# Performance work log

Measured on AMD Instinct MI355X. Metric: run time of the kernel, lower is better.

Reference implementation:

```python
import jax, jax.numpy as jnp
from jax import lax
import numpy as np

B, DIM, H, W = 8, 192, 128, 128
HEADS = 4


def setup_inputs() -> dict:
    key = jax.random.key(0)
    k1, k2, k3, k4 = jax.random.split(key, 4)
    x = jax.random.normal(k1, (B, DIM, H, W), dtype=jnp.float32)
    w_qkv = jax.random.normal(k2, (2 * DIM, DIM), dtype=jnp.float32) * 0.05
    w_dw = jax.random.normal(k3, (2 * DIM, 1, 3, 3), dtype=jnp.float32) * 0.1
    w_proj = jax.random.normal(k4, (DIM, DIM), dtype=jnp.float32) * 0.05
    temperature = jnp.ones((HEADS, 1, 1), dtype=jnp.float32)
    return {"x": x, "w_qkv": w_qkv, "w_dw": w_dw, "w_proj": w_proj, "temperature": temperature}


def reference(x, w_qkv, w_dw, w_proj, temperature):
    b, c, h, w = x.shape
    heads = temperature.shape[0]
    head_c = c // heads
    # 1x1 conv: dim -> 2*dim
    qkv = jnp.einsum('oc,bchw->bohw', w_qkv, x)
    # 3x3 depthwise conv over 2*dim channels
    qkv = lax.conv_general_dilated(
        qkv, w_dw, window_strides=(1, 1), padding='SAME',
        feature_group_count=2 * c,
        dimension_numbers=('NCHW', 'OIHW', 'NCHW'))
    q, v = jnp.split(qkv, 2, axis=1)
    # [b, heads, head_c, h*w]
    q = q.reshape(b, heads, head_c, h * w)
    v = v.reshape(b, heads, head_c, h * w)
    # L2-normalize q over spatial dim; k = q
    q = q / jnp.linalg.norm(q, axis=-1, keepdims=True)
    # channel-wise attention: [b, heads, head_c, head_c]
    attn = jnp.einsum('bhcn,bhdn->bhcd', q, q) * temperature[None]
    attn = jax.nn.softmax(attn, axis=-1)
    out = jnp.einsum('bhcd,bhdn->bhcn', attn, v)
    out = out.reshape(b, c, h, w)
    # 1x1 projection
    return jnp.einsum('oc,bchw->bohw', w_proj, out)
```

## Files before the change

### kernel.cpp

```cpp
#include <hip/hip_runtime.h>

#define BB 8
#define CC 192
#define C2 384
#define HH 128
#define WW 128
#define NN 16384
#define NHEADS 4
#define HC 48
#define LTK 196
#define LTK2 98

typedef float f32x4 __attribute__((ext_vector_type(4)));
typedef float f32x16 __attribute__((ext_vector_type(16)));
typedef short s16x4 __attribute__((ext_vector_type(4)));
typedef short s16x8 __attribute__((ext_vector_type(8)));
typedef unsigned short u16;
typedef u16 u16x4 __attribute__((ext_vector_type(4)));
typedef u16 u16x8 __attribute__((ext_vector_type(8)));
typedef unsigned int u32;

__device__ __forceinline__ float bfu2f(u32 u16v) {
  return __uint_as_float(u16v << 16);
}
__device__ __forceinline__ u16 f2bfu(float f) {
  u32 u = __float_as_uint(f);
  return (u16)((u + 0x7fffu + ((u >> 16) & 1u)) >> 16);
}
__device__ __forceinline__ s16x8 ldpair(const u16* p) {
  s16x4 lo = *reinterpret_cast<const s16x4*>(p);
  s16x4 hi = *reinterpret_cast<const s16x4*>(p + 16);
  return __builtin_shufflevector(lo, hi, 0, 1, 2, 3, 4, 5, 6, 7);
}
__device__ __forceinline__ s16x8 ldb64pair(const u32* p) {
  s16x4 lo = *reinterpret_cast<const s16x4*>(p);
  s16x4 hi = *reinterpret_cast<const s16x4*>(p + 2);
  return __builtin_shufflevector(lo, hi, 0, 1, 2, 3, 4, 5, 6, 7);
}

__global__ __launch_bounds__(256) void k0_wcvt(const float* __restrict__ w,
                                               u16* __restrict__ wbf) {
  const int i = (blockIdx.x * 256 + threadIdx.x) * 4;
  f32x4 v = *reinterpret_cast<const f32x4*>(&w[i]);
  u16x4 o;
  o[0] = f2bfu(v[0]); o[1] = f2bfu(v[1]); o[2] = f2bfu(v[2]); o[3] = f2bfu(v[3]);
  *reinterpret_cast<u16x4*>(&wbf[i]) = o;
}

__global__ __launch_bounds__(512, 4) void k1_qkv(
    const float* __restrict__ x, const u16* __restrict__ wbf,
    u16* __restrict__ qkv) {
  const int n0 = blockIdx.x * 128;
  const int b  = blockIdx.y;
  __shared__ u16 Xs[128 * LTK];
  u32* Xsw = reinterpret_cast<u32*>(Xs);
  const int t = threadIdx.x, lane = t & 63;
  const int wid = t >> 6, wo = wid >> 1, wn = wid & 1;
  const int l31 = lane & 31, g2 = lane >> 5;

  {
    const int nq = t & 31, cr = t >> 5;
    const int kpb = cr >> 1;
    const int jh = cr & 1;
    const int prA = 2 * nq + jh;
    const int prB = 64 + 2 * nq + jh;
    const float* xb = x + (size_t)b * CC * NN + n0 + 4 * nq;
    #pragma unroll 6
    for (int i = 0; i < 12; ++i) {
      f32x4 v = *reinterpret_cast<const f32x4*>(xb + (size_t)(cr + 16 * i) * NN);
      u32 A  = (u32)f2bfu(v[0]) | ((u32)f2bfu(v[1]) << 16);
      u32 Bp = (u32)f2bfu(v[2]) | ((u32)f2bfu(v[3]) << 16);
      u32 oA = __shfl_xor(A, 32);
      u32 oB = __shfl_xor(Bp, 32);
      u32 va, vb;
      if (jh) {
        va = (oB & 0xffffu) | (Bp << 16);
        vb = (oB >> 16) | (Bp & 0xffff0000u);
      } else {
        va = (A & 0xffffu) | (oA << 16);
        vb = (A >> 16) | (oA & 0xffff0000u);
      }
      const int col = kpb + 8 * i;
      Xsw[prA * LTK2 + col] = va;
      Xsw[prB * LTK2 + col] = vb;
    }
  }
  __syncthreads();

  const int nb2 = wn * 32;
  const u32* browE = &Xsw[(nb2 + l31) * LTK2 + 4 * g2];
  const u32* browO = &Xsw[(64 + nb2 + l31) * LTK2 + 4 * g2];

  for (int ot = 0; ot < 3; ++ot) {
    const int o0 = ot * 128;
    const u16* wr = wbf + (size_t)(o0 + wo * 32 + l31) * CC + 8 * g2;
    f32x16 accE, accO;
    #pragma unroll
    for (int e = 0; e < 16; ++e) { accE[e] = 0.f; accO[e] = 0.f; }

    s16x8 af0 = *reinterpret_cast<const s16x8*>(wr);
    s16x8 af1 = *reinterpret_cast<const s16x8*>(wr + 16);
    #pragma unroll
    for (int s = 0; s < 6; ++s) {
      s16x8 an0, an1;
      if (s < 5) {
        an0 = *reinterpret_cast<const s16x8*>(wr + (s + 1) * 32);
        an1 = *reinterpret_cast<const s16x8*>(wr + (s + 1) * 32 + 16);
      }
      s16x8 bfE0 = ldb64pair(browE + 16 * s);
      s16x8 bfE1 = ldb64pair(browE + 16 * s + 8);
      s16x8 bfO0 = ldb64pair(browO + 16 * s);
      s16x8 bfO1 = ldb64pair(browO + 16 * s + 8);
      accE = __builtin_amdgcn_mfma_f32_32x32x16_bf16(af0, bfE0, accE, 0, 0, 0);
      accO = __builtin_amdgcn_mfma_f32_32x32x16_bf16(af0, bfO0, accO, 0, 0, 0);
      accE = __builtin_amdgcn_mfma_f32_32x32x16_bf16(af1, bfE1, accE, 0, 0, 0);
      accO = __builtin_amdgcn_mfma_f32_32x32x16_bf16(af1, bfO1, accO, 0, 0, 0);
      af0 = an0; af1 = an1;
    }
    #pragma unroll
    for (int r = 0; r < 16; ++r) {
      const int row = (r & 3) + 8 * (r >> 2) + 4 * g2;
      const u32 pk = (u32)f2bfu(accE[r]) | ((u32)f2bfu(accO[r]) << 16);
      *reinterpret_cast<u32*>(
          &qkv[((size_t)b * C2 + o0 + wo * 32 + row) * NN + n0 + wn * 64 + 2 * l31]) = pk;
    }
  }
}

__global__ __launch_bounds__(256) void k2_dw(
    const u16* __restrict__ qkv, const float* __restrict__ wdw,
    u16* __restrict__ out) {
  const int gid = blockIdx.x;
  const int rb = gid & 7;
  const int plane = gid >> 3;
  const int ch = plane % C2;
  const int t = threadIdx.x;
  const int row = rb * 16 + (t >> 4);
  const int x0 = (t & 15) * 8;
  const u16* p = qkv + (size_t)plane * NN;
  const float* wv = wdw + ch * 9;
  float o[8];
  #pragma unroll
  for (int j = 0; j < 8; ++j) o[j] = 0.f;
  #pragma unroll
  for (int dy = 0; dy < 3; ++dy) {
    const int yy = row + dy - 1;
    if ((unsigned)yy < (unsigned)HH) {
      const u16* rp = p + yy * WW;
      u16x8 m = *reinterpret_cast<const u16x8*>(&rp[x0]);
      float px[10];
      px[0] = (x0 > 0) ? bfu2f(rp[x0 - 1]) : 0.f;
      px[9] = (x0 < 120) ? bfu2f(rp[x0 + 8]) : 0.f;
      #pragma unroll
      for (int j = 0; j < 8; ++j) px[j + 1] = bfu2f(m[j]);
      const float w0 = wv[dy * 3 + 0], w1 = wv[dy * 3 + 1], w2 = wv[dy * 3 + 2];
      #pragma unroll
      for (int j = 0; j < 8; ++j)
        o[j] += w0 * px[j] + w1 * px[j + 1] + w2 * px[j + 2];
    }
  }
  u16x8 ov;
  #pragma unroll
  for (int j = 0; j < 8; ++j) ov[j] = f2bfu(o[j]);
  *reinterpret_cast<u16x8*>(&out[(size_t)plane * NN + row * WW + x0]) = ov;
}

__global__ __launch_bounds__(256) void k3_gram(
    const u16* __restrict__ qkvd, float* __restrict__ gpart) {
  const int bh = blockIdx.x, b = bh >> 2, h = bh & 3;
  const int chunk = blockIdx.y;
  const int t = threadIdx.x, lane = t & 63, wv = t >> 6;
  const int l15 = lane & 15, g = lane >> 4;
  __shared__ float red[4][2304];
  const u16* qb = qkvd + ((size_t)b * C2 + h * HC) * NN;

  f32x4 acc[3][3];
  #pragma unroll
  for (int i = 0; i < 3; ++i)
    #pragma unroll
    for (int j = 0; j < 3; ++j)
      #pragma unroll
      for (int e = 0; e < 4; ++e) acc[i][j][e] = 0.f;

  const int nbase = chunk * 1024 + wv * 256;
  #pragma unroll 2
  for (int st = 0; st < 8; ++st) {
    const int n = nbase + st * 32;
    s16x8 cf[3];
    #pragma unroll
    for (int i = 0; i < 3; ++i)
      cf[i] = ldpair(qb + (size_t)(i * 16 + l15) * NN + n + 4 * g);
    #pragma unroll
    for (int i = 0; i < 3; ++i)
      #pragma unroll
      for (int j = 0; j < 3; ++j)
        acc[i][j] = __builtin_amdgcn_mfma_f32_16x16x32_bf16(cf[i], cf[j], acc[i][j], 0, 0, 0);
  }
  #pragma unroll
  for (int i = 0; i < 3; ++i)
    #pragma unroll
    for (int j = 0; j < 3; ++j)
      #pragma unroll
      for (int r = 0; r < 4; ++r)
        red[wv][(i * 16 + 4 * g + r) * 48 + j * 16 + l15] = acc[i][j][r];
  __syncthreads();
  float* gp = gpart + ((size_t)bh * 16 + chunk) * 2304;
  for (int idx = t; idx < 2304; idx += 256)
    gp[idx] = red[0][idx] + red[1][idx] + red[2][idx] + red[3][idx];
}

__global__ __launch_bounds__(256) void k4_soft(
    const float* __restrict__ gpart, const float* __restrict__ temp,
    float* __restrict__ attn) {
  const int bh = blockIdx.x;
  const int h = bh & 3;
  const int t = threadIdx.x;
  __shared__ float G[2304];
  __shared__ float rn[48];
  for (int idx = t; idx < 2304; idx += 256) {
    float s = 0.f;
    #pragma unroll
    for (int c = 0; c < 16; ++c) s += gpart[((size_t)bh * 16 + c) * 2304 + idx];
    G[idx] = s;
  }
  __syncthreads();
  if (t < 48) rn[t] = rsqrtf(G[t * 48 + t]);
  __syncthreads();
  if (t < 48) {
    const float tm = temp[h];
    float v[48];
    float mx = -1e30f;
    #pragma unroll
    for (int j = 0; j < 48; ++j) {
      v[j] = G[t * 48 + j] * rn[t] * rn[j] * tm;
      mx = fmaxf(mx, v[j]);
    }
    float s = 0.f;
    #pragma unroll
    for (int j = 0; j < 48; ++j) { v[j] = expf(v[j] - mx); s += v[j]; }
    const float inv = 1.f / s;
    #pragma unroll
    for (int j = 0; j < 48; ++j)
      attn[(size_t)bh * 2304 + t * 48 + j] = v[j] * inv;
  }
}

__global__ __launch_bounds__(192) void k5_M(
    const float* __restrict__ wproj, const float* __restrict__ attn,
    u16* __restrict__ Mbf) {
  const int o = blockIdx.x;
  const int b = blockIdx.y;
  const int d = threadIdx.x;
  const int h = d / HC, dl = d % HC;
  const float* wrow = wproj + o * CC + h * HC;
  const float* at = attn + ((size_t)(b * NHEADS + h)) * 2304;
  float s = 0.f;
  #pragma unroll
  for (int c = 0; c < HC; ++c) s = fmaf(wrow[c], at[c * HC + dl], s);
  Mbf[((size_t)b * CC + o) * CC + d] = f2bfu(s);
}

__global__ __launch_bounds__(256, 4) void k6_out(
    const u16* __restrict__ Mbf, const u16* __restrict__ qkvd,
    float* __restrict__ out) {
  const int n0 = blockIdx.x * 128;
  const int b  = blockIdx.y;
  __shared__ u16 Vs[128 * LTK];
  u32* Vsw = reinterpret_cast<u32*>(Vs);
  const int t = threadIdx.x, lane = t & 63;
  const int wid = t >> 6, wo = wid >> 1, wn = wid & 1;
  const int l31 = lane & 31, g2 = lane >> 5;

  {
    const int nq = t & 31, cr = t >> 5;
    const int kpb = cr >> 1;
    const int jh = cr & 1;
    const int prA = 2 * nq + jh;
    const int prB = 64 + 2 * nq + jh;
    const u16* vbp = qkvd + ((size_t)b * C2 + CC) * NN + n0 + 4 * nq;
    #pragma unroll 6
    for (int i = 0; i < 24; ++i) {
      u16x4 m = *reinterpret_cast<const u16x4*>(vbp + (size_t)(cr + 8 * i) * NN);
      u32 A  = (u32)m[0] | ((u32)m[1] << 16);
      u32 Bp = (u32)m[2] | ((u32)m[3] << 16);
      u32 oA = __shfl_xor(A, 32);
      u32 oB = __shfl_xor(Bp, 32);
      u32 va, vb;
      if (jh) {
        va = (oB & 0xffffu) | (Bp << 16);
        vb = (oB >> 16) | (Bp & 0xffff0000u);
      } else {
        va = (A & 0xffffu) | (oA << 16);
        vb = (A >> 16) | (oA & 0xffff0000u);
      }
      const int col = kpb + 4 * i;
      Vsw[prA * LTK2 + col] = va;
      Vsw[prB * LTK2 + col] = vb;
    }
  }
  __syncthreads();

  const int nb2 = wn * 32;
  const u32* browE = &Vsw[(nb2 + l31) * LTK2 + 4 * g2];
  const u32* browO = &Vsw[(64 + nb2 + l31) * LTK2 + 4 * g2];
  const u16* Ab = Mbf + (size_t)b * CC * CC;

  for (int ot = 0; ot < 3; ++ot) {
    const int o0 = ot * 64;
    const u16* ar = Ab + (size_t)(o0 + wo * 32 + l31) * CC + 8 * g2;
    f32x16 accE, accO;
    #pragma unroll
    for (int e = 0; e < 16; ++e) { accE[e] = 0.f; accO[e] = 0.f; }

    s16x8 af0 = *reinterpret_cast<const s16x8*>(ar);
    s16x8 af1 = *reinterpret_cast<const s16x8*>(ar + 16);
    #pragma unroll
    for (int s = 0; s < 6; ++s) {
      s16x8 an0, an1;
      if (s < 5) {
        an0 = *reinterpret_cast<const s16x8*>(ar + (s + 1) * 32);
        an1 = *reinterpret_cast<const s16x8*>(ar + (s + 1) * 32 + 16);
      }
      s16x8 bfE0 = ldb64pair(browE + 16 * s);
      s16x8 bfE1 = ldb64pair(browE + 16 * s + 8);
      s16x8 bfO0 = ldb64pair(browO + 16 * s);
      s16x8 bfO1 = ldb64pair(browO + 16 * s + 8);
      accE = __builtin_amdgcn_mfma_f32_32x32x16_bf16(af0, bfE0, accE, 0, 0, 0);
      accO = __builtin_amdgcn_mfma_f32_32x32x16_bf16(af0, bfO0, accO, 0, 0, 0);
      accE = __builtin_amdgcn_mfma_f32_32x32x16_bf16(af1, bfE1, accE, 0, 0, 0);
      accO = __builtin_amdgcn_mfma_f32_32x32x16_bf16(af1, bfO1, accO, 0, 0, 0);
      af0 = an0; af1 = an1;
    }
    #pragma unroll
    for (int r = 0; r < 16; ++r) {
      const int row = (r & 3) + 8 * (r >> 2) + 4 * g2;
      float2 st;
      st.x = accE[r];
      st.y = accO[r];
      *reinterpret_cast<float2*>(
          &out[((size_t)b * CC + o0 + wo * 32 + row) * NN + n0 + wn * 64 + 2 * l31]) = st;
    }
  }
}

extern "C" void kernel_launch(void* const* d_in, const int* in_sizes, int n_in,
                              void* d_out, int out_size, void* d_ws, size_t ws_size,
                              hipStream_t stream) {
  const float* x      = (const float*)d_in[0];
  const float* w_qkv  = (const float*)d_in[1];
  const float* w_dw   = (const float*)d_in[2];
  const float* w_proj = (const float*)d_in[3];
  const float* temp   = (const float*)d_in[4];
  float* out = (float*)d_out;

  const size_t OFF_QKV   = 0;
  const size_t OFF_QKVD  = 100663296ULL;
  const size_t OFF_GPART = 201326592ULL;
  const size_t OFF_ATTN  = 206045184ULL;
  const size_t OFF_M     = 206340096ULL;
  const size_t OFF_WBF   = 206929920ULL;
  const size_t NEEDED    = 207077376ULL;
  if (ws_size < NEEDED) return;

  char* ws = (char*)d_ws;
  u16* qkv   = (u16*)(ws + OFF_QKV);
  u16* qkvd  = (u16*)(ws + OFF_QKVD);
  float* gpart = (float*)(ws + OFF_GPART);
  float* attn  = (float*)(ws + OFF_ATTN);
  u16* Mbf   = (u16*)(ws + OFF_M);
  u16* wbf   = (u16*)(ws + OFF_WBF);

  k0_wcvt<<<dim3(72), 256, 0, stream>>>(w_qkv, wbf);
  k1_qkv <<<dim3(128, 8), 512, 0, stream>>>(x, wbf, qkv);
  k2_dw  <<<dim3(BB * C2 * 8), 256, 0, stream>>>(qkv, w_dw, qkvd);
  k3_gram<<<dim3(BB * NHEADS, 16), 256, 0, stream>>>(qkvd, gpart);
  k4_soft<<<dim3(BB * NHEADS), 256, 0, stream>>>(gpart, temp, attn);
  k5_M   <<<dim3(CC, BB), 192, 0, stream>>>(w_proj, attn, Mbf);
  k6_out <<<dim3(128, 8), 256, 0, stream>>>(Mbf, qkvd, out);
}
```

Baseline: 213.2 us.

## Fuse q depthwise conv into Gram kernel and restrict dw conv to v

The depthwise conv for the q half is now computed on the fly inside the Gram kernel from LDS-staged pre-conv rows (with halo), so the dw kernel only handles the v channels. This avoids writing and re-reading the convolved q tensor. The conv work moves into the Gram kernel, which raises its ALU load and LDS use, and it repeats redundant per-lane scalar LDS reads. Block indices in the qkv and output kernels are also swizzled to change spatial tile order.

```diff
diff --git a/kernel.cpp b/kernel.cpp
--- a/kernel.cpp
+++ b/kernel.cpp
@@ -50,7 +50,8 @@
 __global__ __launch_bounds__(512, 4) void k1_qkv(
     const float* __restrict__ x, const u16* __restrict__ wbf,
     u16* __restrict__ qkv) {
-  const int n0 = blockIdx.x * 128;
+  const int bx = blockIdx.x;
+  const int n0 = (((bx & 7) << 4) + (bx >> 3)) << 7;
   const int b  = blockIdx.y;
   __shared__ u16 Xs[128 * LTK];
   u32* Xsw = reinterpret_cast<u32*>(Xs);
@@ -132,12 +133,14 @@
     u16* __restrict__ out) {
   const int gid = blockIdx.x;
   const int rb = gid & 7;
-  const int plane = gid >> 3;
-  const int ch = plane % C2;
+  const int p = gid >> 3;
+  const int b = p / 192, cv = p % 192;
+  const int ch = CC + cv;
+  const int plane = b * C2 + ch;
   const int t = threadIdx.x;
   const int row = rb * 16 + (t >> 4);
   const int x0 = (t & 15) * 8;
-  const u16* p = qkv + (size_t)plane * NN;
+  const u16* pp = qkv + (size_t)plane * NN;
   const float* wv = wdw + ch * 9;
   float o[8];
   #pragma unroll
@@ -146,7 +149,7 @@
   for (int dy = 0; dy < 3; ++dy) {
     const int yy = row + dy - 1;
     if ((unsigned)yy < (unsigned)HH) {
-      const u16* rp = p + yy * WW;
+      const u16* rp = pp + yy * WW;
       u16x8 m = *reinterpret_cast<const u16x8*>(&rp[x0]);
       float px[10];
       px[0] = (x0 > 0) ? bfu2f(rp[x0 - 1]) : 0.f;
@@ -165,14 +168,25 @@
   *reinterpret_cast<u16x8*>(&out[(size_t)plane * NN + row * WW + x0]) = ov;
 }
 
-__global__ __launch_bounds__(256) void k3_gram(
-    const u16* __restrict__ qkvd, float* __restrict__ gpart) {
-  const int bh = blockIdx.x, b = bh >> 2, h = bh & 3;
-  const int chunk = blockIdx.y;
+__global__ __launch_bounds__(256, 2) void k23_convgram(
+    const u16* __restrict__ qkv, const float* __restrict__ wdw,
+    float* __restrict__ gpart) {
+  const int rgRaw = blockIdx.x;
+  const int rg = ((rgRaw & 7) << 1) + (rgRaw >> 3);
+  const int h = blockIdx.y, b = blockIdx.z;
+  const int bh = b * NHEADS + h;
+  __shared__ u16 inq[48 * 776];
   const int t = threadIdx.x, lane = t & 63, wv = t >> 6;
   const int l15 = lane & 15, g = lane >> 4;
-  __shared__ float red[4][2304];
-  const u16* qb = qkvd + ((size_t)b * C2 + h * HC) * NN;
+  const u16* qb = qkv + ((size_t)b * C2 + h * HC) * NN;
+
+  float wc[3][9];
+  #pragma unroll
+  for (int i = 0; i < 3; ++i) {
+    const float* wp = wdw + (h * HC + i * 16 + l15) * 9;
+    #pragma unroll
+    for (int e = 0; e < 9; ++e) wc[i][e] = wp[e];
+  }
 
   f32x4 acc[3][3];
   #pragma unroll
@@ -182,31 +196,77 @@
       #pragma unroll
       for (int e = 0; e < 4; ++e) acc[i][j][e] = 0.f;
 
-  const int nbase = chunk * 1024 + wv * 256;
-  #pragma unroll 2
-  for (int st = 0; st < 8; ++st) {
-    const int n = nbase + st * 32;
-    s16x8 cf[3];
-    #pragma unroll
-    for (int i = 0; i < 3; ++i)
-      cf[i] = ldpair(qb + (size_t)(i * 16 + l15) * NN + n + 4 * g);
-    #pragma unroll
-    for (int i = 0; i < 3; ++i)
-      #pragma unroll
-      for (int j = 0; j < 3; ++j)
-        acc[i][j] = __builtin_amdgcn_mfma_f32_16x16x32_bf16(cf[i], cf[j], acc[i][j], 0, 0, 0);
-  }
+  for (int ck = 0; ck < 2; ++ck) {
+    const int R0 = rg * 8 + ck * 4;
+    __syncthreads();
+    #pragma unroll 3
+    for (int i = 0; i < 18; ++i) {
+      const int idx = t + 256 * i;
+      const int ch = idx / 96, grp = idx % 96;
+      const int gn = (R0 - 1) * 128 + grp * 8;
+      u16x8 v;
+      #pragma unroll
+      for (int e = 0; e < 8; ++e) v[e] = 0;
+      if (gn >= 0 && gn < NN)
+        v = *reinterpret_cast<const u16x8*>(qb + (size_t)ch * NN + gn);
+      *reinterpret_cast<u16x8*>(&inq[ch * 776 + grp * 8]) = v;
+    }
+    __syncthreads();
+
+    #pragma unroll
+    for (int s = 0; s < 4; ++s) {
+      s16x8 cf[3];
+      #pragma unroll
+      for (int i = 0; i < 3; ++i) {
+        const u16* cbase = &inq[(i * 16 + l15) * 776];
+        u16 o8[8];
+        #pragma unroll
+        for (int half = 0; half < 2; ++half) {
+          const int n = wv * 128 + s * 32 + half * 16 + 4 * g;
+          const int row = n >> 7, x0 = n & 127;
+          const int br = row + 1;
+          #pragma unroll
+          for (int j = 0; j < 4; ++j) {
+            float sum = 0.f;
+            #pragma unroll
+            for (int dy = 0; dy < 3; ++dy) {
+              const u16* rp = cbase + (br + dy - 1) * 128;
+              #pragma unroll
+              for (int dx = 0; dx < 3; ++dx) {
+                const int xx = x0 + j + dx - 1;
+                if (0 <= xx && xx < 128)
+                  sum += wc[i][dy * 3 + dx] * bfu2f(rp[xx]);
+              }
+            }
+            o8[half * 4 + j] = f2bfu(sum);
+          }
+        }
+        s16x8 f;
+        #pragma unroll
+        for (int e = 0; e < 8; ++e) f[e] = (short)o8[e];
+        cf[i] = f;
+      }
+      #pragma unroll
+      for (int i = 0; i < 3; ++i)
+        #pragma unroll
+        for (int j = 0; j < 3; ++j)
+          acc[i][j] = __builtin_amdgcn_mfma_f32_16x16x32_bf16(cf[i], cf[j], acc[i][j], 0, 0, 0);
+    }
+  }
+
+  __syncthreads();
+  float* red = reinterpret_cast<float*>(inq);
   #pragma unroll
   for (int i = 0; i < 3; ++i)
     #pragma unroll
     for (int j = 0; j < 3; ++j)
       #pragma unroll
       for (int r = 0; r < 4; ++r)
-        red[wv][(i * 16 + 4 * g + r) * 48 + j * 16 + l15] = acc[i][j][r];
-  __syncthreads();
-  float* gp = gpart + ((size_t)bh * 16 + chunk) * 2304;
+        red[wv * 2304 + (i * 16 + 4 * g + r) * 48 + j * 16 + l15] = acc[i][j][r];
+  __syncthreads();
+  float* gp = gpart + ((size_t)bh * 16 + rg) * 2304;
   for (int idx = t; idx < 2304; idx += 256)
-    gp[idx] = red[0][idx] + red[1][idx] + red[2][idx] + red[3][idx];
+    gp[idx] = red[idx] + red[2304 + idx] + red[4608 + idx] + red[6912 + idx];
 }
 
 __global__ __launch_bounds__(256) void k4_soft(
@@ -263,7 +323,8 @@
 __global__ __launch_bounds__(256, 4) void k6_out(
     const u16* __restrict__ Mbf, const u16* __restrict__ qkvd,
     float* __restrict__ out) {
-  const int n0 = blockIdx.x * 128;
+  const int bx = blockIdx.x;
+  const int n0 = (((bx & 7) << 4) + (bx >> 3)) << 7;
   const int b  = blockIdx.y;
   __shared__ u16 Vs[128 * LTK];
   u32* Vsw = reinterpret_cast<u32*>(Vs);
@@ -372,8 +433,8 @@
 
   k0_wcvt<<<dim3(72), 256, 0, stream>>>(w_qkv, wbf);
   k1_qkv <<<dim3(128, 8), 512, 0, stream>>>(x, wbf, qkv);
-  k2_dw  <<<dim3(BB * C2 * 8), 256, 0, stream>>>(qkv, w_dw, qkvd);
-  k3_gram<<<dim3(BB * NHEADS, 16), 256, 0, stream>>>(qkvd, gpart);
+  k2_dw  <<<dim3(BB * 192 * 8), 256, 0, stream>>>(qkv, w_dw, qkvd);
+  k23_convgram<<<dim3(16, NHEADS, BB), 256, 0, stream>>>(qkv, w_dw, gpart);
   k4_soft<<<dim3(BB * NHEADS), 256, 0, stream>>>(gpart, temp, attn);
   k5_M   <<<dim3(CC, BB), 192, 0, stream>>>(w_proj, attn, Mbf);
   k6_out <<<dim3(128, 8), 256, 0, stream>>>(Mbf, qkvd, out);
```

Result: slower. 283.0 us (+32.7%).
